# Kernel tuning notes

Hardware: AMD Instinct MI355X
Metric: run time of the kernel (lower is better)

Reference implementation:

```python
import jax, jax.numpy as jnp
import numpy as np

B, N, D_IN = 8, 8192, 13
RATIO, R, K = 0.25, 0.2, 32


def setup_inputs() -> dict:
    key = jax.random.key(0)
    k1, k2, k3, k4 = jax.random.split(key, 4)
    x = jax.random.normal(k1, (B, N, D_IN), dtype=jnp.float32)
    pos = jax.random.uniform(k2, (B, N, 3), dtype=jnp.float32)
    batch = jnp.broadcast_to(jnp.arange(B, dtype=jnp.int32)[:, None], (B, N))
    W1 = jax.random.normal(k3, (D_IN + 3, 64), dtype=jnp.float32) * 0.1
    b1 = jnp.zeros((64,), jnp.float32)
    W2 = jax.random.normal(k4, (64, 128), dtype=jnp.float32) * 0.1
    b2 = jnp.zeros((128,), jnp.float32)
    return {"x": x, "pos": pos, "batch": batch, "W1": W1, "b1": b1, "W2": W2, "b2": b2}


def _fps_single(p, M):
    """Deterministic farthest point sampling (start at index 0). p: [N,3] -> [M] int32."""
    n = p.shape[0]

    def step(carry, _):
        mind, last = carry
        d = jnp.sum((p - p[last]) ** 2, axis=-1)
        mind = jnp.minimum(mind, d)
        nxt = jnp.argmax(mind).astype(jnp.int32)
        return (mind, nxt), nxt

    init = (jnp.full((n,), 1e10, p.dtype), jnp.int32(0))
    _, rest = jax.lax.scan(step, init, None, length=M - 1)
    return jnp.concatenate([jnp.zeros((1,), jnp.int32), rest])


def reference(x, pos, batch, W1, b1, W2, b2):
    M = int(RATIO * N)
    # --- FPS per cloud ---
    idx = jax.vmap(lambda p: _fps_single(p, M))(pos)              # [B, M]
    pos_s = jnp.take_along_axis(pos, idx[..., None], axis=1)      # [B, M, 3]
    # --- radius ball query: first K in-ball neighbors by point index ---
    d2 = jnp.sum((pos_s[:, :, None, :] - pos[:, None, :, :]) ** 2, axis=-1)  # [B, M, N]
    within = d2 <= R * R
    rank = jnp.where(within, jnp.arange(N, dtype=jnp.int32), N)   # invalid -> N
    negv, nbr = jax.lax.top_k(-rank, K)                           # K smallest ranks
    valid = negv > -N                                             # [B, M, K]
    # --- gather -> local_nn MLP -> masked max-scatter (PointNetConv) ---
    x_j = jax.vmap(lambda a, i: a[i])(x, nbr)                     # [B, M, K, D_IN]
    pos_j = jax.vmap(lambda a, i: a[i])(pos, nbr)                 # [B, M, K, 3]
    feat = jnp.concatenate([x_j, pos_j - pos_s[:, :, None, :]], axis=-1)
    h = jax.nn.relu(feat @ W1 + b1)
    h = jax.nn.relu(h @ W2 + b2)                                  # [B, M, K, 128]
    h = jnp.where(valid[..., None], h, -jnp.inf)
    x_out = jnp.max(h, axis=2)                                    # [B, M, 128]
    batch_s = jnp.take_along_axis(batch, idx, axis=1)             # [B, M]
    return x_out, pos_s, batch_s
```

## Files before the change

kernel.cpp:

```cpp
#include <hip/hip_runtime.h>
#include <cstddef>

#define B_   8
#define N_   8192
#define M_   2048
#define K_   32
#define DIN_ 13

typedef _Float16 f16x8 __attribute__((ext_vector_type(8)));
typedef float    f32x4 __attribute__((ext_vector_type(4)));

template <int CTRL>
__device__ __forceinline__ float dppmax(float v) {
  int o = __builtin_amdgcn_update_dpp(
      (int)0xff800000, __float_as_int(v), CTRL, 0xF, 0xF, false);
  return fmaxf(v, __int_as_float(o));
}
template <int CTRL>
__device__ __forceinline__ float dppminf(float v) {
  int o = __builtin_amdgcn_update_dpp(
      (int)0x7f800000, __float_as_int(v), CTRL, 0xF, 0xF, false);
  return fminf(v, __int_as_float(o));
}
__device__ __forceinline__ float wave_reduce_max(float v) {
  v = dppmax<0x111>(v); v = dppmax<0x112>(v); v = dppmax<0x114>(v);
  v = dppmax<0x118>(v); v = dppmax<0x142>(v); v = dppmax<0x143>(v);
  return __int_as_float(__builtin_amdgcn_readlane(__float_as_int(v), 63));
}
__device__ __forceinline__ float wave_reduce_min(float v) {
  v = dppminf<0x111>(v); v = dppminf<0x112>(v); v = dppminf<0x114>(v);
  v = dppminf<0x118>(v); v = dppminf<0x142>(v); v = dppminf<0x143>(v);
  return __int_as_float(__builtin_amdgcn_readlane(__float_as_int(v), 63));
}

__global__ __launch_bounds__(1024, 4) void fps_kernel(
    const float* __restrict__ pos,
    float* __restrict__ pos_s,
    float* __restrict__ batch_s)
{
  const int b = blockIdx.x;
  const int t = threadIdx.x;
  const float* p = pos + (size_t)b * N_ * 3;

  __shared__ float px_l[N_], py_l[N_], pz_l[N_];
  __shared__ int   r2o[N_];
  __shared__ int   vbase[64];
  __shared__ int   vcur[64];
  __shared__ unsigned long long kslot[3];

  for (int mm = t; mm < M_; mm += 1024)
    batch_s[b * M_ + mm] = (float)b;
  if (t < 64) vcur[t] = 0;
  if (t == 0) { kslot[0] = 0ull; kslot[1] = 0ull; kslot[2] = 0ull; }
  __syncthreads();

  int vid[8];
#pragma unroll
  for (int i = 0; i < 8; ++i) {
    int j = t + 1024 * i;
    float x = p[j * 3 + 0], y = p[j * 3 + 1], z = p[j * 3 + 2];
    px_l[j] = x; py_l[j] = y; pz_l[j] = z;
    int ix = (int)(x * 4.f); ix = ix < 0 ? 0 : (ix > 3 ? 3 : ix);
    int iy = (int)(y * 4.f); iy = iy < 0 ? 0 : (iy > 3 ? 3 : iy);
    int iz = (int)(z * 4.f); iz = iz < 0 ? 0 : (iz > 3 ? 3 : iz);
    int v = (ix & 1) | ((iy & 1) << 1) | ((iz & 1) << 2) |
            ((ix >> 1) << 3) | ((iy >> 1) << 4) | ((iz >> 1) << 5);
    vid[i] = v;
    atomicAdd(&vcur[v], 1);
  }
  __syncthreads();

  if (t < 64) {
    int h = vcur[t]; int sc = h;
#pragma unroll
    for (int d = 1; d < 64; d <<= 1) {
      int o = __shfl_up(sc, d);
      if (t >= d) sc += o;
    }
    vbase[t] = sc - h;
    vcur[t]  = 0;
  }
  __syncthreads();

#pragma unroll
  for (int i = 0; i < 8; ++i) {
    int j = t + 1024 * i;
    int r = vbase[vid[i]] + atomicAdd(&vcur[vid[i]], 1);
    r2o[r] = j;
  }
  __syncthreads();

  float px[8], py[8], pz[8], mind[8]; int oi[8];
#pragma unroll
  for (int i = 0; i < 8; ++i) {
    int o = r2o[t * 8 + i];
    oi[i] = o;
    px[i] = px_l[o]; py[i] = py_l[o]; pz[i] = pz_l[o];
    mind[i] = 1e10f;
  }
#pragma unroll
  for (int i = 0; i < 8; ++i) {
    asm volatile("" : "+v"(px[i]), "+v"(py[i]), "+v"(pz[i]));
  }

  float mnx = px[0], mxx = px[0], mny = py[0], mxy = py[0],
        mnz = pz[0], mxz = pz[0];
#pragma unroll
  for (int i = 1; i < 8; ++i) {
    mnx = fminf(mnx, px[i]); mxx = fmaxf(mxx, px[i]);
    mny = fminf(mny, py[i]); mxy = fmaxf(mxy, py[i]);
    mnz = fminf(mnz, pz[i]); mxz = fmaxf(mxz, pz[i]);
  }
  const float bxmin = wave_reduce_min(mnx), bxmax = wave_reduce_max(mxx);
  const float bymin = wave_reduce_min(mny), bymax = wave_reduce_max(mxy);
  const float bzmin = wave_reduce_min(mnz), bzmax = wave_reduce_max(mxz);

  float lx = px_l[0], ly = py_l[0], lz = pz_l[0];
  if (t == 0) {
    pos_s[(size_t)b * M_ * 3 + 0] = lx;
    pos_s[(size_t)b * M_ * 3 + 1] = ly;
    pos_s[(size_t)b * M_ * 3 + 2] = lz;
  }

  float wtm = 1e10f;
  float cwm = 0.f;
  unsigned int cjc = 0xFFFFFFFFu;
  int sl = 1;
  int rs = 0;

  for (int s = 1; s < M_; ++s) {
    float cx = fmaxf(fmaxf(bxmin - lx, lx - bxmax), 0.f);
    float cy = fmaxf(fmaxf(bymin - ly, ly - bymax), 0.f);
    float cz = fmaxf(fmaxf(bzmin - lz, lz - bzmax), 0.f);
    float LB = (cx * cx + cy * cy) + cz * cz;
    bool proc = (LB * 0.999999f < wtm);

    if (proc) {
      float tmax;
      {
#pragma clang fp contract(off)
#pragma unroll
        for (int i = 0; i < 8; ++i) {
          float dx = px[i] - lx, dy = py[i] - ly, dz = pz[i] - lz;
          float d  = (dx * dx + dy * dy) + dz * dz;
          mind[i]  = fminf(mind[i], d);
        }
        float m0 = fmaxf(mind[0], mind[1]), m1 = fmaxf(mind[2], mind[3]);
        float m2 = fmaxf(mind[4], mind[5]), m3 = fmaxf(mind[6], mind[7]);
        tmax = fmaxf(fmaxf(m0, m1), fmaxf(m2, m3));
      }
      const float wm = wave_reduce_max(tmax);
      wtm = wm;
      cwm = wm;
      unsigned int cc = 0xFFFFFFFFu;
#pragma unroll
      for (int i = 0; i < 8; ++i) {
        unsigned int cand = (mind[i] == wm) ? (unsigned int)oi[i] : 0xFFFFFFFFu;
        cc = cc < cand ? cc : cand;
      }
      cjc = cc;
    }
    if (cjc != 0xFFFFFFFFu) {
      unsigned long long key =
          ((unsigned long long)__float_as_uint(cwm) << 32) |
          (unsigned long long)(0xFFFFFFFFu - cjc);
      atomicMax(&kslot[sl], key);
    }
    __syncthreads();
    if (t == 0) kslot[rs] = 0ull;
    const unsigned long long kk = kslot[sl];
    const int wj  = (int)(0xFFFFFFFFu - (unsigned int)(kk & 0xFFFFFFFFull));
    const int wju = (int)__builtin_amdgcn_readfirstlane(wj);
    lx = px_l[wju]; ly = py_l[wju]; lz = pz_l[wju];
    if (t == 0) {
      size_t o2 = ((size_t)b * M_ + s) * 3;
      pos_s[o2 + 0] = lx; pos_s[o2 + 1] = ly; pos_s[o2 + 2] = lz;
    }
    sl = (sl == 2) ? 0 : sl + 1;
    rs = (rs == 2) ? 0 : rs + 1;
  }
}

__global__ __launch_bounds__(256) void prep_kernel(
    const float* __restrict__ W1, const float* __restrict__ W2,
    _Float16* __restrict__ w1t, _Float16* __restrict__ w2t)
{
  int t = blockIdx.x * 256 + threadIdx.x;
  if (t < 8192) {
    int n = t >> 6, k = t & 63;
    w2t[t] = (_Float16)W2[k * 128 + n];
  }
  int u = t - 8192;
  if (u >= 0 && u < 1024) {
    int n = u >> 4, k = u & 15;
    w1t[u] = (_Float16)W1[k * 64 + n];
  }
}

__global__ __launch_bounds__(64) void sa_kernel(
    const float* __restrict__ x,
    const float* __restrict__ pos,
    const float* __restrict__ b1,
    const float* __restrict__ b2,
    const float* __restrict__ pos_s,
    const _Float16* __restrict__ w1t,
    const _Float16* __restrict__ w2t,
    float* __restrict__ x_out)
{
  const int blk  = blockIdx.x;
  const int b    = blk >> 11;
  const int m    = blk & 2047;
  const int lane = threadIdx.x;
  const int l15  = lane & 15;
  const int quad = lane >> 4;

  __shared__ int      nbr[K_];
  __shared__ _Float16 featb[K_][24];
  __shared__ _Float16 h1b[K_][72];

  const float* pb = pos + (size_t)b * N_ * 3;
  const float* xb = x   + (size_t)b * N_ * DIN_;
  const size_t so = ((size_t)b * M_ + m) * 3;
  const float sx = pos_s[so + 0];
  const float sy = pos_s[so + 1];
  const float sz = pos_s[so + 2];
  const float R2 = (float)(0.2 * 0.2);

  int cnt = 0;
  for (int base = 0; base < N_ && cnt < K_; base += 64) {
    int j = base + lane;
    float qx = pb[j * 3 + 0], qy = pb[j * 3 + 1], qz = pb[j * 3 + 2];
    bool win;
    {
#pragma clang fp contract(off)
      float dx = sx - qx, dy = sy - qy, dz = sz - qz;
      float d2 = (dx * dx + dy * dy) + dz * dz;
      win = d2 <= R2;
    }
    unsigned long long mk = __ballot(win);
    int rank = (int)__popcll(mk & ((1ull << lane) - 1ull));
    if (win) {
      int slot = cnt + rank;
      if (slot < K_) nbr[slot] = j;
    }
    cnt += (int)__popcll(mk);
  }
  const int valid = cnt < K_ ? cnt : K_;
  __syncthreads();

  for (int tq = lane; tq < K_ * 16; tq += 64) {
    int r = tq >> 4, i = tq & 15;
    float v = 0.f;
    if (r < valid) {
      int j = nbr[r];
      if (i < DIN_) {
        v = xb[j * DIN_ + i];
      } else {
        float c = (i == 13) ? sx : (i == 14) ? sy : sz;
        float q = pb[j * 3 + (i - 13)];
        v = q - c;
      }
    }
    featb[r][i] = (_Float16)v;
  }
  __syncthreads();

  f16x8 fz;
#pragma unroll
  for (int i = 0; i < 8; ++i) fz[i] = (_Float16)0;

  f16x8 a1[2], b1f[4];
#pragma unroll
  for (int mt = 0; mt < 2; ++mt)
    a1[mt] = (quad < 2) ? *(const f16x8*)&featb[mt * 16 + l15][quad * 8] : fz;
#pragma unroll
  for (int nt = 0; nt < 4; ++nt)
    b1f[nt] = (quad < 2) ? *(const f16x8*)&w1t[(nt * 16 + l15) * 16 + quad * 8]
                         : fz;

#pragma unroll
  for (int mt = 0; mt < 2; ++mt) {
#pragma unroll
    for (int nt = 0; nt < 4; ++nt) {
      f32x4 c = {0.f, 0.f, 0.f, 0.f};
      c = __builtin_amdgcn_mfma_f32_16x16x32_f16(a1[mt], b1f[nt], c, 0, 0, 0);
      float bb = b1[nt * 16 + l15];
#pragma unroll
      for (int r = 0; r < 4; ++r) {
        float v = c[r] + bb;
        h1b[mt * 16 + quad * 4 + r][nt * 16 + l15] =
            (_Float16)(v > 0.f ? v : 0.f);
      }
    }
  }
  __syncthreads();

  f16x8 a2[2][2];
#pragma unroll
  for (int mt = 0; mt < 2; ++mt)
#pragma unroll
    for (int kt = 0; kt < 2; ++kt)
      a2[mt][kt] = *(const f16x8*)&h1b[mt * 16 + l15][kt * 32 + quad * 8];

  float* o = x_out + ((size_t)b * M_ + m) * 128;
#pragma unroll
  for (int nt = 0; nt < 8; ++nt) {
    f16x8 b20 = *(const f16x8*)&w2t[(nt * 16 + l15) * 64 + 0 * 32 + quad * 8];
    f16x8 b21 = *(const f16x8*)&w2t[(nt * 16 + l15) * 64 + 1 * 32 + quad * 8];
    f32x4 c0 = {0.f, 0.f, 0.f, 0.f}, c1 = {0.f, 0.f, 0.f, 0.f};
    c0 = __builtin_amdgcn_mfma_f32_16x16x32_f16(a2[0][0], b20, c0, 0, 0, 0);
    c0 = __builtin_amdgcn_mfma_f32_16x16x32_f16(a2[0][1], b21, c0, 0, 0, 0);
    c1 = __builtin_amdgcn_mfma_f32_16x16x32_f16(a2[1][0], b20, c1, 0, 0, 0);
    c1 = __builtin_amdgcn_mfma_f32_16x16x32_f16(a2[1][1], b21, c1, 0, 0, 0);
    float bv = b2[nt * 16 + l15];
    float acc = -INFINITY;
#pragma unroll
    for (int r = 0; r < 4; ++r) {
      int row0 = quad * 4 + r;
      int row1 = 16 + quad * 4 + r;
      float v0 = c0[r] + bv; v0 = v0 > 0.f ? v0 : 0.f;
      float v1 = c1[r] + bv; v1 = v1 > 0.f ? v1 : 0.f;
      if (row0 < valid) acc = fmaxf(acc, v0);
      if (row1 < valid) acc = fmaxf(acc, v1);
    }
    acc = fmaxf(acc, __shfl_xor(acc, 16));
    acc = fmaxf(acc, __shfl_xor(acc, 32));
    if (quad == 0) o[nt * 16 + l15] = acc;
  }
}

extern "C" void kernel_launch(void* const* d_in, const int* in_sizes, int n_in,
                              void* d_out, int out_size, void* d_ws, size_t ws_size,
                              hipStream_t stream) {
  (void)in_sizes; (void)n_in; (void)ws_size; (void)out_size;
  const float* x   = (const float*)d_in[0];
  const float* pos = (const float*)d_in[1];
  const float* W1  = (const float*)d_in[3];
  const float* b1  = (const float*)d_in[4];
  const float* W2  = (const float*)d_in[5];
  const float* b2  = (const float*)d_in[6];

  float* out     = (float*)d_out;
  float* x_out   = out;
  float* pos_s   = out + (size_t)B_ * M_ * 128;
  float* batch_s = pos_s + (size_t)B_ * M_ * 3;

  _Float16* w1t = (_Float16*)d_ws;
  _Float16* w2t = w1t + 1024;

  prep_kernel<<<36, 256, 0, stream>>>(W1, W2, w1t, w2t);
  fps_kernel<<<B_, 1024, 0, stream>>>(pos, pos_s, batch_s);
  sa_kernel<<<B_ * M_, 64, 0, stream>>>(x, pos, b1, b2, pos_s, w1t, w2t, x_out);
}
```

Baseline: 1.718 ms.

## Refine FPS pruning to per-thread bounds with finer 512-voxel spatial sort

The spatial sort of points goes from 64 voxels to 512 (8x8x8), with a two-level scan to build voxel offsets. Pruning now uses per-thread bounding boxes (8 points each) instead of per-wave boxes, so each thread keeps its own lower-bound test and a wave skips the update only when no lane needs it. Candidate indices are reduced inside the wave, and only lane 0 issues the LDS atomicMax, which cuts atomic traffic per step. The aim is to skip more distance updates in the serial FPS loop, at the cost of a ballot and an extra DPP min reduction per processed step.

```diff
diff --git a/kernel.cpp b/kernel.cpp
--- a/kernel.cpp
+++ b/kernel.cpp
@@ -22,15 +22,21 @@
       (int)0x7f800000, __float_as_int(v), CTRL, 0xF, 0xF, false);
   return fminf(v, __int_as_float(o));
 }
+template <int CTRL>
+__device__ __forceinline__ unsigned dppminu(unsigned v) {
+  unsigned o = (unsigned)__builtin_amdgcn_update_dpp(
+      (int)0xFFFFFFFF, (int)v, CTRL, 0xF, 0xF, false);
+  return v < o ? v : o;
+}
 __device__ __forceinline__ float wave_reduce_max(float v) {
   v = dppmax<0x111>(v); v = dppmax<0x112>(v); v = dppmax<0x114>(v);
   v = dppmax<0x118>(v); v = dppmax<0x142>(v); v = dppmax<0x143>(v);
   return __int_as_float(__builtin_amdgcn_readlane(__float_as_int(v), 63));
 }
-__device__ __forceinline__ float wave_reduce_min(float v) {
-  v = dppminf<0x111>(v); v = dppminf<0x112>(v); v = dppminf<0x114>(v);
-  v = dppminf<0x118>(v); v = dppminf<0x142>(v); v = dppminf<0x143>(v);
-  return __int_as_float(__builtin_amdgcn_readlane(__float_as_int(v), 63));
+__device__ __forceinline__ unsigned wave_reduce_min_u32(unsigned v) {
+  v = dppminu<0x111>(v); v = dppminu<0x112>(v); v = dppminu<0x114>(v);
+  v = dppminu<0x118>(v); v = dppminu<0x142>(v); v = dppminu<0x143>(v);
+  return (unsigned)__builtin_amdgcn_readlane((int)v, 63);
 }
 
 __global__ __launch_bounds__(1024, 4) void fps_kernel(
@@ -38,19 +44,22 @@
     float* __restrict__ pos_s,
     float* __restrict__ batch_s)
 {
-  const int b = blockIdx.x;
-  const int t = threadIdx.x;
+  const int b    = blockIdx.x;
+  const int t    = threadIdx.x;
+  const int lane = t & 63;
+  const int wid  = t >> 6;
   const float* p = pos + (size_t)b * N_ * 3;
 
   __shared__ float px_l[N_], py_l[N_], pz_l[N_];
   __shared__ int   r2o[N_];
-  __shared__ int   vbase[64];
-  __shared__ int   vcur[64];
+  __shared__ int   vbase[512];
+  __shared__ int   vcur[512];
+  __shared__ int   wsum[8];
   __shared__ unsigned long long kslot[3];
 
   for (int mm = t; mm < M_; mm += 1024)
     batch_s[b * M_ + mm] = (float)b;
-  if (t < 64) vcur[t] = 0;
+  if (t < 512) vcur[t] = 0;
   if (t == 0) { kslot[0] = 0ull; kslot[1] = 0ull; kslot[2] = 0ull; }
   __syncthreads();
 
@@ -60,26 +69,40 @@
     int j = t + 1024 * i;
     float x = p[j * 3 + 0], y = p[j * 3 + 1], z = p[j * 3 + 2];
     px_l[j] = x; py_l[j] = y; pz_l[j] = z;
-    int ix = (int)(x * 4.f); ix = ix < 0 ? 0 : (ix > 3 ? 3 : ix);
-    int iy = (int)(y * 4.f); iy = iy < 0 ? 0 : (iy > 3 ? 3 : iy);
-    int iz = (int)(z * 4.f); iz = iz < 0 ? 0 : (iz > 3 ? 3 : iz);
+    int ix = (int)(x * 8.f); ix = ix < 0 ? 0 : (ix > 7 ? 7 : ix);
+    int iy = (int)(y * 8.f); iy = iy < 0 ? 0 : (iy > 7 ? 7 : iy);
+    int iz = (int)(z * 8.f); iz = iz < 0 ? 0 : (iz > 7 ? 7 : iz);
     int v = (ix & 1) | ((iy & 1) << 1) | ((iz & 1) << 2) |
-            ((ix >> 1) << 3) | ((iy >> 1) << 4) | ((iz >> 1) << 5);
+            (((ix >> 1) & 1) << 3) | (((iy >> 1) & 1) << 4) |
+            (((iz >> 1) & 1) << 5) |
+            ((ix >> 2) << 6) | ((iy >> 2) << 7) | ((iz >> 2) << 8);
     vid[i] = v;
     atomicAdd(&vcur[v], 1);
   }
   __syncthreads();
 
-  if (t < 64) {
-    int h = vcur[t]; int sc = h;
+  int h = 0, sc = 0;
+  if (t < 512) {
+    h = vcur[t]; sc = h;
 #pragma unroll
     for (int d = 1; d < 64; d <<= 1) {
       int o = __shfl_up(sc, d);
-      if (t >= d) sc += o;
-    }
-    vbase[t] = sc - h;
-    vcur[t]  = 0;
-  }
+      if (lane >= d) sc += o;
+    }
+    if (lane == 63) wsum[wid] = sc;
+  }
+  __syncthreads();
+  if (t < 8) {
+    int v = wsum[t]; int inc = v;
+#pragma unroll
+    for (int d = 1; d < 8; d <<= 1) {
+      int o = __shfl_up(inc, d);
+      if (t >= d) inc += o;
+    }
+    wsum[t] = inc - v;
+  }
+  __syncthreads();
+  if (t < 512) { vbase[t] = sc - h + wsum[t >> 6]; vcur[t] = 0; }
   __syncthreads();
 
 #pragma unroll
@@ -103,17 +126,14 @@
     asm volatile("" : "+v"(px[i]), "+v"(py[i]), "+v"(pz[i]));
   }
 
-  float mnx = px[0], mxx = px[0], mny = py[0], mxy = py[0],
-        mnz = pz[0], mxz = pz[0];
+  float bxmin = px[0], bxmax = px[0], bymin = py[0], bymax = py[0],
+        bzmin = pz[0], bzmax = pz[0];
 #pragma unroll
   for (int i = 1; i < 8; ++i) {
-    mnx = fminf(mnx, px[i]); mxx = fmaxf(mxx, px[i]);
-    mny = fminf(mny, py[i]); mxy = fmaxf(mxy, py[i]);
-    mnz = fminf(mnz, pz[i]); mxz = fmaxf(mxz, pz[i]);
-  }
-  const float bxmin = wave_reduce_min(mnx), bxmax = wave_reduce_max(mxx);
-  const float bymin = wave_reduce_min(mny), bymax = wave_reduce_max(mxy);
-  const float bzmin = wave_reduce_min(mnz), bzmax = wave_reduce_max(mxz);
+    bxmin = fminf(bxmin, px[i]); bxmax = fmaxf(bxmax, px[i]);
+    bymin = fminf(bymin, py[i]); bymax = fmaxf(bymax, py[i]);
+    bzmin = fminf(bzmin, pz[i]); bzmax = fmaxf(bzmax, pz[i]);
+  }
 
   float lx = px_l[0], ly = py_l[0], lz = pz_l[0];
   if (t == 0) {
@@ -122,9 +142,9 @@
     pos_s[(size_t)b * M_ * 3 + 2] = lz;
   }
 
-  float wtm = 1e10f;
+  float ltm = 1e10f;
   float cwm = 0.f;
-  unsigned int cjc = 0xFFFFFFFFu;
+  unsigned cmin = 0xFFFFFFFFu;
   int sl = 1;
   int rs = 0;
 
@@ -133,9 +153,8 @@
     float cy = fmaxf(fmaxf(bymin - ly, ly - bymax), 0.f);
     float cz = fmaxf(fmaxf(bzmin - lz, lz - bzmax), 0.f);
     float LB = (cx * cx + cy * cy) + cz * cz;
-    bool proc = (LB * 0.999999f < wtm);
-
-    if (proc) {
+    bool lp = (LB * 0.999999f < ltm);
+    if (__ballot(lp) != 0ull) {
       float tmax;
       {
 #pragma clang fp contract(off)
@@ -149,21 +168,21 @@
         float m2 = fmaxf(mind[4], mind[5]), m3 = fmaxf(mind[6], mind[7]);
         tmax = fmaxf(fmaxf(m0, m1), fmaxf(m2, m3));
       }
+      ltm = tmax;
       const float wm = wave_reduce_max(tmax);
-      wtm = wm;
       cwm = wm;
-      unsigned int cc = 0xFFFFFFFFu;
+      unsigned cc = 0xFFFFFFFFu;
 #pragma unroll
       for (int i = 0; i < 8; ++i) {
-        unsigned int cand = (mind[i] == wm) ? (unsigned int)oi[i] : 0xFFFFFFFFu;
+        unsigned cand = (mind[i] == wm) ? (unsigned)oi[i] : 0xFFFFFFFFu;
         cc = cc < cand ? cc : cand;
       }
-      cjc = cc;
-    }
-    if (cjc != 0xFFFFFFFFu) {
+      cmin = wave_reduce_min_u32(cc);
+    }
+    if (lane == 0) {
       unsigned long long key =
           ((unsigned long long)__float_as_uint(cwm) << 32) |
-          (unsigned long long)(0xFFFFFFFFu - cjc);
+          (unsigned long long)(0xFFFFFFFFu - cmin);
       atomicMax(&kslot[sl], key);
     }
     __syncthreads();
```

After: 1.503 ms. 12.5% less time.
